# Performance work log

Measured on AMD Instinct MI355X. Metric: run time of the kernel, lower is better.

The kernel has to match this reference:

```python
import jax, jax.numpy as jnp
import numpy as np

N_AGENTS = 32
STATE_DIM = 512
EMBED = 64
BATCH = 32768


def setup_inputs() -> dict:
    key = jax.random.key(0)
    ks = jax.random.split(key, 16)
    g = lambda k, shape, fan_in: jax.random.normal(k, shape, jnp.float32) / np.sqrt(fan_in)
    return {
        "agent_qs": jax.random.normal(ks[0], (BATCH, N_AGENTS), jnp.float32),
        "states": jax.random.normal(ks[1], (BATCH, STATE_DIM), jnp.float32),
        # hyper_w1: Linear(state,E) -> ReLU -> Linear(E, n_agents*E)
        "w1_l1_w": g(ks[2], (EMBED, STATE_DIM), STATE_DIM),
        "w1_l1_b": jnp.zeros((EMBED,), jnp.float32),
        "w1_l2_w": g(ks[3], (N_AGENTS * EMBED, EMBED), EMBED),
        "w1_l2_b": jnp.zeros((N_AGENTS * EMBED,), jnp.float32),
        # hyper_w2: Linear(state,E) -> ReLU -> Linear(E, E)
        "w2_l1_w": g(ks[4], (EMBED, STATE_DIM), STATE_DIM),
        "w2_l1_b": jnp.zeros((EMBED,), jnp.float32),
        "w2_l2_w": g(ks[5], (EMBED, EMBED), EMBED),
        "w2_l2_b": jnp.zeros((EMBED,), jnp.float32),
        # hyper_b1: Linear(state, E)
        "b1_w": g(ks[6], (EMBED, STATE_DIM), STATE_DIM),
        "b1_b": jnp.zeros((EMBED,), jnp.float32),
        # hyper_b2: Linear(state,E) -> ReLU -> Linear(E, 1)
        "b2_l1_w": g(ks[7], (EMBED, STATE_DIM), STATE_DIM),
        "b2_l1_b": jnp.zeros((EMBED,), jnp.float32),
        "b2_l2_w": g(ks[8], (1, EMBED), EMBED),
        "b2_l2_b": jnp.zeros((1,), jnp.float32),
    }


def _linear(x, w, b):
    return x @ w.T + b


def reference(agent_qs, states,
              w1_l1_w, w1_l1_b, w1_l2_w, w1_l2_b,
              w2_l1_w, w2_l1_b, w2_l2_w, w2_l2_b,
              b1_w, b1_b, b2_l1_w, b2_l1_b, b2_l2_w, b2_l2_b):
    B = agent_qs.shape[0]
    # hypernetworks producing per-sample weights
    w1 = jnp.abs(_linear(jax.nn.relu(_linear(states, w1_l1_w, w1_l1_b)), w1_l2_w, w1_l2_b))
    w1 = w1.reshape(B, N_AGENTS, EMBED)                      # [B, A, E]
    b1 = _linear(states, b1_w, b1_b)                         # [B, E]
    hidden = jax.nn.elu(jnp.einsum('ba,bae->be', agent_qs, w1) + b1)  # [B, E]
    w2 = jnp.abs(_linear(jax.nn.relu(_linear(states, w2_l1_w, w2_l1_b)), w2_l2_w, w2_l2_b))  # [B, E]
    b2 = _linear(jax.nn.relu(_linear(states, b2_l1_w, b2_l1_b)), b2_l2_w, b2_l2_b)           # [B, 1]
    q_total = jnp.einsum('be,be->b', hidden, w2) + b2[:, 0]  # [B]
    return q_total
```

## Files before the change

kernel.cpp:

```cpp
#include <hip/hip_runtime.h>

typedef unsigned short u16;
typedef unsigned int u32;
typedef short bf16x8 __attribute__((ext_vector_type(8)));
typedef float f32x4 __attribute__((ext_vector_type(4)));
typedef u16 u16x4 __attribute__((ext_vector_type(4)));

#define NAG 32
#define STATE 512
#define EMBED 64
#define TB 64

#define OFF_W1L1 0
#define OFF_W2L1 32768
#define OFF_B1W  65536
#define OFF_B2L1 98304
#define OFF_W1L2 131072
#define OFF_W2L2 262144
#define WS_TOTAL 266240

__device__ __forceinline__ float bf2f(u16 u) {
    u32 i = ((u32)u) << 16; float f;
    __builtin_memcpy(&f, &i, 4); return f;
}
__device__ __forceinline__ u16 f2bf(float f) {
    u32 i; __builtin_memcpy(&i, &f, 4);
    return (u16)((i + 0x8000u) >> 16);
}
__device__ __forceinline__ bf16x8 ld8(const u16* p) {
    return *reinterpret_cast<const bf16x8*>(p);
}
__device__ __forceinline__ bf16x8 cvt8(f32x4 a, f32x4 b) {
    bf16x8 r;
#pragma unroll
    for (int i = 0; i < 4; ++i) r[i]     = (short)f2bf(a[i]);
#pragma unroll
    for (int i = 0; i < 4; ++i) r[i + 4] = (short)f2bf(b[i]);
    return r;
}

__global__ __launch_bounds__(256) void cvt_weights(
    const float* __restrict__ w1l1w, const float* __restrict__ w2l1w,
    const float* __restrict__ b1w,   const float* __restrict__ b2l1w,
    const float* __restrict__ w1l2w, const float* __restrict__ w2l2w,
    u16* __restrict__ ws)
{
    int idx = blockIdx.x * 256 + threadIdx.x;
    const float* src; int off;
    if      (idx < OFF_W2L1)  { src = w1l1w; off = OFF_W1L1; }
    else if (idx < OFF_B1W)   { src = w2l1w; off = OFF_W2L1; }
    else if (idx < OFF_B2L1)  { src = b1w;   off = OFF_B1W;  }
    else if (idx < OFF_W1L2)  { src = b2l1w; off = OFF_B2L1; }
    else if (idx < OFF_W2L2)  { src = w1l2w; off = OFF_W1L2; }
    else if (idx < WS_TOTAL)  { src = w2l2w; off = OFF_W2L2; }
    else return;
    ws[idx] = f2bf(src[idx - off]);
}

__global__ __launch_bounds__(256, 2) void qmix_kernel(
    const float* __restrict__ qs,    const float* __restrict__ st,
    const u16*  __restrict__ wsb,
    const float* __restrict__ w1l1b, const float* __restrict__ w1l2b,
    const float* __restrict__ w2l1b, const float* __restrict__ w2l2b,
    const float* __restrict__ b1b,   const float* __restrict__ b2l1b,
    const float* __restrict__ b2l2w, const float* __restrict__ b2l2b,
    float* __restrict__ out)
{
    __shared__ u16  y[TB][264];
    __shared__ u16  pbuf[4][TB][68];
    __shared__ u16  qst[NAG][68];
    __shared__ u16  w1bs[2048];
    __shared__ float qacc[TB];
    __shared__ float b2wv[64];

    const int t    = threadIdx.x;
    const int wave = t >> 6, lane = t & 63;
    const int m = lane & 15, quad = lane >> 4;
    const int sbase = blockIdx.x * TB;

    if (t < 64) b2wv[t] = b2l2w[t];
    {
        const float* qp = qs + (size_t)sbase * NAG + t * 8;
        f32x4 q0 = *reinterpret_cast<const f32x4*>(qp);
        f32x4 q1 = *reinterpret_cast<const f32x4*>(qp + 4);
        const int s = t >> 2, a0 = (t & 3) * 8;
#pragma unroll
        for (int j = 0; j < 4; ++j) qst[a0 + j][s]     = f2bf(q0[j]);
#pragma unroll
        for (int j = 0; j < 4; ++j) qst[a0 + 4 + j][s] = f2bf(q1[j]);
        f32x4 w0 = *reinterpret_cast<const f32x4*>(w1l2b + t * 8);
        f32x4 w1 = *reinterpret_cast<const f32x4*>(w1l2b + t * 8 + 4);
        *reinterpret_cast<bf16x8*>(&w1bs[t * 8]) = cvt8(w0, w1);
    }

    const u16*   wArow = wsb + (size_t)(wave * 64) * STATE;
    const float* stb   = st + (size_t)sbase * STATE;

    f32x4 acc[4][4] = {};
    for (int ks = 0; ks < 8; ++ks) {
        bf16x8 b[4][2];
#pragma unroll
        for (int ot = 0; ot < 4; ++ot) {
            const u16* wr = wArow + (size_t)(ot * 16 + m) * STATE + ks * 64 + quad * 8;
            b[ot][0] = ld8(wr);
            b[ot][1] = ld8(wr + 32);
        }
#pragma unroll
        for (int st2 = 0; st2 < 4; ++st2) {
            const float* ap = stb + (size_t)(st2 * 16 + m) * STATE + ks * 64 + quad * 8;
            f32x4 a0 = *reinterpret_cast<const f32x4*>(ap);
            f32x4 a1 = *reinterpret_cast<const f32x4*>(ap + 4);
            f32x4 a2 = *reinterpret_cast<const f32x4*>(ap + 32);
            f32x4 a3 = *reinterpret_cast<const f32x4*>(ap + 36);
            bf16x8 af0 = cvt8(a0, a1);
            bf16x8 af1 = cvt8(a2, a3);
#pragma unroll
            for (int ot = 0; ot < 4; ++ot)
                acc[st2][ot] = __builtin_amdgcn_mfma_f32_16x16x32_bf16(af0, b[ot][0], acc[st2][ot], 0, 0, 0);
#pragma unroll
            for (int ot = 0; ot < 4; ++ot)
                acc[st2][ot] = __builtin_amdgcn_mfma_f32_16x16x32_bf16(af1, b[ot][1], acc[st2][ot], 0, 0, 0);
        }
    }
    {
        const float* barr = (wave == 0) ? w1l1b : (wave == 1) ? w2l1b : (wave == 2) ? b1b : b2l1b;
        const bool isrelu = (wave != 2);
        float wb[4];
#pragma unroll
        for (int ot = 0; ot < 4; ++ot) wb[ot] = barr[ot * 16 + m];
#pragma unroll
        for (int st2 = 0; st2 < 4; ++st2)
#pragma unroll
            for (int ot = 0; ot < 4; ++ot)
#pragma unroll
                for (int r = 0; r < 4; ++r) {
                    float v = acc[st2][ot][r] + wb[ot];
                    if (isrelu) v = fmaxf(v, 0.f);
                    y[st2 * 16 + quad * 4 + r][wave * 64 + ot * 16 + m] = f2bf(v);
                }
    }
    __syncthreads();

    bf16x8 h1f[4][2];
#pragma unroll
    for (int st2 = 0; st2 < 4; ++st2) {
        h1f[st2][0] = *reinterpret_cast<const bf16x8*>(&y[st2 * 16 + m][quad * 8]);
        h1f[st2][1] = *reinterpret_cast<const bf16x8*>(&y[st2 * 16 + m][32 + quad * 8]);
    }

    f32x4 hacc[4][4] = {};
    for (int ag = 0; ag < 8; ++ag) {
        const int a = wave * 8 + ag;
        const u16* wp = wsb + OFF_W1L2 + (size_t)a * 64 * EMBED;
        bf16x8 b[4][2];
#pragma unroll
        for (int ot = 0; ot < 4; ++ot) {
            const u16* wr = wp + (size_t)(ot * 16 + m) * EMBED + quad * 8;
            b[ot][0] = ld8(wr);
            b[ot][1] = ld8(wr + 32);
        }
        float bias[4];
#pragma unroll
        for (int ot = 0; ot < 4; ++ot) bias[ot] = bf2f(w1bs[a * EMBED + ot * 16 + m]);
#pragma unroll
        for (int st2 = 0; st2 < 4; ++st2) {
            u16x4 qv = *reinterpret_cast<const u16x4*>(&qst[a][st2 * 16 + quad * 4]);
#pragma unroll
            for (int ot = 0; ot < 4; ++ot) {
                f32x4 p = {};
                p = __builtin_amdgcn_mfma_f32_16x16x32_bf16(h1f[st2][0], b[ot][0], p, 0, 0, 0);
                p = __builtin_amdgcn_mfma_f32_16x16x32_bf16(h1f[st2][1], b[ot][1], p, 0, 0, 0);
#pragma unroll
                for (int r = 0; r < 4; ++r)
                    hacc[st2][ot][r] += bf2f((u16)qv[r]) * fabsf(p[r] + bias[ot]);
            }
        }
    }
#pragma unroll
    for (int st2 = 0; st2 < 4; ++st2)
#pragma unroll
        for (int ot = 0; ot < 4; ++ot)
#pragma unroll
            for (int r = 0; r < 4; ++r)
                pbuf[wave][st2 * 16 + quad * 4 + r][ot * 16 + m] = f2bf(hacc[st2][ot][r]);
    __syncthreads();

    {
        const int s  = wave * 16 + (lane & 15);
        const int eb = (lane >> 4) * 16;
        float v[16];
#pragma unroll
        for (int j = 0; j < 16; ++j) v[j] = 0.f;
#pragma unroll
        for (int pw = 0; pw < 4; ++pw) {
#pragma unroll
            for (int c = 0; c < 4; ++c) {
                u16x4 x = *reinterpret_cast<const u16x4*>(&pbuf[pw][s][eb + c * 4]);
#pragma unroll
                for (int j = 0; j < 4; ++j) v[c * 4 + j] += bf2f((u16)x[j]);
            }
        }
        bf16x8 bv0 = *reinterpret_cast<const bf16x8*>(&y[s][128 + eb]);
        bf16x8 bv1 = *reinterpret_cast<const bf16x8*>(&y[s][128 + eb + 8]);
        bf16x8 o0, o1;
#pragma unroll
        for (int j = 0; j < 8; ++j) {
            float h0 = v[j] + bf2f((u16)bv0[j]);
            h0 = (h0 > 0.f) ? h0 : (__expf(h0) - 1.f);
            o0[j] = (short)f2bf(h0);
            float h1 = v[8 + j] + bf2f((u16)bv1[j]);
            h1 = (h1 > 0.f) ? h1 : (__expf(h1) - 1.f);
            o1[j] = (short)f2bf(h1);
        }
        *reinterpret_cast<bf16x8*>(&y[s][128 + eb])     = o0;
        *reinterpret_cast<bf16x8*>(&y[s][128 + eb + 8]) = o1;
    }
    __syncthreads();

    const int s0 = wave * 16;
    bf16x8 h2f0 = *reinterpret_cast<const bf16x8*>(&y[s0 + m][64 + quad * 8]);
    bf16x8 h2f1 = *reinterpret_cast<const bf16x8*>(&y[s0 + m][96 + quad * 8]);

    f32x4 qp = {};
#pragma unroll
    for (int tp = 0; tp < 4; ++tp) {
        const u16* wc = wsb + OFF_W2L2 + (size_t)(tp * 16 + m) * EMBED + quad * 8;
        bf16x8 b0 = ld8(wc);
        bf16x8 b1 = ld8(wc + 32);
        f32x4 p = {};
        p = __builtin_amdgcn_mfma_f32_16x16x32_bf16(h2f0, b0, p, 0, 0, 0);
        p = __builtin_amdgcn_mfma_f32_16x16x32_bf16(h2f1, b1, p, 0, 0, 0);
        const float bias = w2l2b[tp * 16 + m];
#pragma unroll
        for (int r = 0; r < 4; ++r)
            qp[r] += bf2f(y[s0 + quad * 4 + r][128 + tp * 16 + m]) * fabsf(p[r] + bias);
    }
#pragma unroll
    for (int off = 1; off < 16; off <<= 1) {
#pragma unroll
        for (int r = 0; r < 4; ++r) qp[r] += __shfl_xor(qp[r], off, 64);
    }
    if (m == 0) {
#pragma unroll
        for (int r = 0; r < 4; ++r) qacc[s0 + quad * 4 + r] = qp[r];
    }
    __syncthreads();

    if (t < TB) {
        float q = qacc[t] + b2l2b[0];
        float acc2 = 0.f;
#pragma unroll
        for (int kk = 0; kk < 8; ++kk) {
            bf16x8 hv = *reinterpret_cast<const bf16x8*>(&y[t][192 + kk * 8]);
#pragma unroll
            for (int j = 0; j < 8; ++j)
                acc2 += bf2f((u16)hv[j]) * b2wv[kk * 8 + j];
        }
        out[sbase + t] = q + acc2;
    }
}

extern "C" void kernel_launch(void* const* d_in, const int* in_sizes, int n_in,
                              void* d_out, int out_size, void* d_ws, size_t ws_size,
                              hipStream_t stream)
{
    const float* qs    = (const float*)d_in[0];
    const float* st    = (const float*)d_in[1];
    const float* w1l1w = (const float*)d_in[2];
    const float* w1l1b = (const float*)d_in[3];
    const float* w1l2w = (const float*)d_in[4];
    const float* w1l2b = (const float*)d_in[5];
    const float* w2l1w = (const float*)d_in[6];
    const float* w2l1b = (const float*)d_in[7];
    const float* w2l2w = (const float*)d_in[8];
    const float* w2l2b = (const float*)d_in[9];
    const float* b1w   = (const float*)d_in[10];
    const float* b1b   = (const float*)d_in[11];
    const float* b2l1w = (const float*)d_in[12];
    const float* b2l1b = (const float*)d_in[13];
    const float* b2l2w = (const float*)d_in[14];
    const float* b2l2b = (const float*)d_in[15];

    u16* wsb = (u16*)d_ws;

    cvt_weights<<<(WS_TOTAL + 255) / 256, 256, 0, stream>>>(
        w1l1w, w2l1w, b1w, b2l1w, w1l2w, w2l2w, wsb);

    int B = in_sizes[0] / NAG;
    int grid = B / TB;
    qmix_kernel<<<grid, 256, 0, stream>>>(
        qs, st, wsb,
        w1l1b, w1l2b, w2l1b, w2l2b, b1b, b2l1b, b2l2w, b2l2b,
        (float*)d_out);
}
```

Baseline: 175.3 us.

## Stage states tile through double-buffered LDS and prefetch weights in both GEMM loops

The states tile is now loaded cooperatively once per k-step, converted to bf16 and stored into a double-buffered LDS region. Previously each wave re-read and re-converted the whole states tile from global memory. Weight fragments for the first GEMM and for the per-agent w1 second layer are register double-buffered, so the next step's loads are in flight during the current MFMAs. The b2 hypernet dot product is folded into wave 3's epilogue with shuffle reductions, and shared memory is packed into one aliased buffer to cut LDS usage. The cost is a barrier per k-step and higher register pressure from the unrolled double buffers.

```diff
diff --git a/kernel.cpp b/kernel.cpp
--- a/kernel.cpp
+++ b/kernel.cpp
@@ -18,6 +18,21 @@
 #define OFF_W1L2 131072
 #define OFF_W2L2 262144
 #define WS_TOTAL 266240
+
+#define Y_STR    200
+#define SB_OFF   12800
+#define SB_STR   72
+#define SB_BUF   (64 * 72)
+#define W1BS_OFF 22016
+#define QST_OFF  24064
+#define QST_STR  68
+#define PBUF_OFF 12800
+#define PBUF_STR 68
+#define PBUF_WV  (64 * 68)
+#define QACC_OFF  30208
+#define QACC2_OFF 30336
+#define B2WV_OFF  30464
+#define SMEM_U16  30592
 
 __device__ __forceinline__ float bf2f(u16 u) {
     u32 i = ((u32)u) << 16; float f;
@@ -66,64 +81,97 @@
     const float* __restrict__ b2l2w, const float* __restrict__ b2l2b,
     float* __restrict__ out)
 {
-    __shared__ u16  y[TB][264];
-    __shared__ u16  pbuf[4][TB][68];
-    __shared__ u16  qst[NAG][68];
-    __shared__ u16  w1bs[2048];
-    __shared__ float qacc[TB];
-    __shared__ float b2wv[64];
+    __shared__ u16 smem[SMEM_U16];
+    float* qaccF  = (float*)(smem + QACC_OFF);
+    float* qacc2F = (float*)(smem + QACC2_OFF);
+    float* b2wvF  = (float*)(smem + B2WV_OFF);
 
     const int t    = threadIdx.x;
     const int wave = t >> 6, lane = t & 63;
     const int m = lane & 15, quad = lane >> 4;
     const int sbase = blockIdx.x * TB;
 
-    if (t < 64) b2wv[t] = b2l2w[t];
+    if (t < 64) b2wvF[t] = b2l2w[t];
     {
         const float* qp = qs + (size_t)sbase * NAG + t * 8;
         f32x4 q0 = *reinterpret_cast<const f32x4*>(qp);
         f32x4 q1 = *reinterpret_cast<const f32x4*>(qp + 4);
         const int s = t >> 2, a0 = (t & 3) * 8;
 #pragma unroll
-        for (int j = 0; j < 4; ++j) qst[a0 + j][s]     = f2bf(q0[j]);
-#pragma unroll
-        for (int j = 0; j < 4; ++j) qst[a0 + 4 + j][s] = f2bf(q1[j]);
+        for (int j = 0; j < 4; ++j) smem[QST_OFF + (a0 + j) * QST_STR + s]     = f2bf(q0[j]);
+#pragma unroll
+        for (int j = 0; j < 4; ++j) smem[QST_OFF + (a0 + 4 + j) * QST_STR + s] = f2bf(q1[j]);
         f32x4 w0 = *reinterpret_cast<const f32x4*>(w1l2b + t * 8);
         f32x4 w1 = *reinterpret_cast<const f32x4*>(w1l2b + t * 8 + 4);
-        *reinterpret_cast<bf16x8*>(&w1bs[t * 8]) = cvt8(w0, w1);
-    }
-
-    const u16*   wArow = wsb + (size_t)(wave * 64) * STATE;
-    const float* stb   = st + (size_t)sbase * STATE;
+        *reinterpret_cast<bf16x8*>(&smem[W1BS_OFF + t * 8]) = cvt8(w0, w1);
+    }
+
+    const int ss1 = t >> 3, c8 = t & 7;
+    const float* stb = st + (size_t)sbase * STATE;
+
+    {
+        const float* g1 = stb + (size_t)ss1 * STATE + c8 * 8;
+        const float* g2 = g1 + (size_t)32 * STATE;
+        f32x4 a0 = *reinterpret_cast<const f32x4*>(g1);
+        f32x4 a1 = *reinterpret_cast<const f32x4*>(g1 + 4);
+        f32x4 a2 = *reinterpret_cast<const f32x4*>(g2);
+        f32x4 a3 = *reinterpret_cast<const f32x4*>(g2 + 4);
+        u16* dst = smem + SB_OFF;
+        *reinterpret_cast<bf16x8*>(&dst[ss1 * SB_STR + c8 * 8])        = cvt8(a0, a1);
+        *reinterpret_cast<bf16x8*>(&dst[(ss1 + 32) * SB_STR + c8 * 8]) = cvt8(a2, a3);
+    }
+
+    const u16* wAw = wsb + (size_t)(wave * 64) * STATE;
+    bf16x8 bfr[2][4][2];
+#pragma unroll
+    for (int ot = 0; ot < 4; ++ot) {
+        const u16* wr = wAw + (size_t)(ot * 16 + m) * STATE + quad * 8;
+        bfr[0][ot][0] = ld8(wr);
+        bfr[0][ot][1] = ld8(wr + 32);
+    }
+    __syncthreads();
 
     f32x4 acc[4][4] = {};
+#pragma unroll
     for (int ks = 0; ks < 8; ++ks) {
-        bf16x8 b[4][2];
-#pragma unroll
-        for (int ot = 0; ot < 4; ++ot) {
-            const u16* wr = wArow + (size_t)(ot * 16 + m) * STATE + ks * 64 + quad * 8;
-            b[ot][0] = ld8(wr);
-            b[ot][1] = ld8(wr + 32);
-        }
+        f32x4 sa0 = {}, sa1 = {}, sa2 = {}, sa3 = {};
+        if (ks < 7) {
+            const float* g1 = stb + (size_t)ss1 * STATE + (ks + 1) * 64 + c8 * 8;
+            const float* g2 = g1 + (size_t)32 * STATE;
+            sa0 = *reinterpret_cast<const f32x4*>(g1);
+            sa1 = *reinterpret_cast<const f32x4*>(g1 + 4);
+            sa2 = *reinterpret_cast<const f32x4*>(g2);
+            sa3 = *reinterpret_cast<const f32x4*>(g2 + 4);
+#pragma unroll
+            for (int ot = 0; ot < 4; ++ot) {
+                const u16* wr = wAw + (size_t)(ot * 16 + m) * STATE + (ks + 1) * 64 + quad * 8;
+                bfr[(ks + 1) & 1][ot][0] = ld8(wr);
+                bfr[(ks + 1) & 1][ot][1] = ld8(wr + 32);
+            }
+        }
+        const u16* sbc = smem + SB_OFF + (ks & 1) * SB_BUF;
 #pragma unroll
         for (int st2 = 0; st2 < 4; ++st2) {
-            const float* ap = stb + (size_t)(st2 * 16 + m) * STATE + ks * 64 + quad * 8;
-            f32x4 a0 = *reinterpret_cast<const f32x4*>(ap);
-            f32x4 a1 = *reinterpret_cast<const f32x4*>(ap + 4);
-            f32x4 a2 = *reinterpret_cast<const f32x4*>(ap + 32);
-            f32x4 a3 = *reinterpret_cast<const f32x4*>(ap + 36);
-            bf16x8 af0 = cvt8(a0, a1);
-            bf16x8 af1 = cvt8(a2, a3);
+            const int row = st2 * 16 + m;
+            bf16x8 af0 = ld8(&sbc[row * SB_STR + quad * 8]);
+            bf16x8 af1 = ld8(&sbc[row * SB_STR + (quad + 4) * 8]);
 #pragma unroll
             for (int ot = 0; ot < 4; ++ot)
-                acc[st2][ot] = __builtin_amdgcn_mfma_f32_16x16x32_bf16(af0, b[ot][0], acc[st2][ot], 0, 0, 0);
+                acc[st2][ot] = __builtin_amdgcn_mfma_f32_16x16x32_bf16(af0, bfr[ks & 1][ot][0], acc[st2][ot], 0, 0, 0);
 #pragma unroll
             for (int ot = 0; ot < 4; ++ot)
-                acc[st2][ot] = __builtin_amdgcn_mfma_f32_16x16x32_bf16(af1, b[ot][1], acc[st2][ot], 0, 0, 0);
-        }
-    }
-    {
-        const float* barr = (wave == 0) ? w1l1b : (wave == 1) ? w2l1b : (wave == 2) ? b1b : b2l1b;
+                acc[st2][ot] = __builtin_amdgcn_mfma_f32_16x16x32_bf16(af1, bfr[ks & 1][ot][1], acc[st2][ot], 0, 0, 0);
+        }
+        if (ks < 7) {
+            u16* dst = smem + SB_OFF + ((ks + 1) & 1) * SB_BUF;
+            *reinterpret_cast<bf16x8*>(&dst[ss1 * SB_STR + c8 * 8])        = cvt8(sa0, sa1);
+            *reinterpret_cast<bf16x8*>(&dst[(ss1 + 32) * SB_STR + c8 * 8]) = cvt8(sa2, sa3);
+        }
+        __syncthreads();
+    }
+
+    if (wave != 3) {
+        const float* barr = (wave == 0) ? w1l1b : (wave == 1) ? w2l1b : b1b;
         const bool isrelu = (wave != 2);
         float wb[4];
 #pragma unroll
@@ -136,53 +184,84 @@
                 for (int r = 0; r < 4; ++r) {
                     float v = acc[st2][ot][r] + wb[ot];
                     if (isrelu) v = fmaxf(v, 0.f);
-                    y[st2 * 16 + quad * 4 + r][wave * 64 + ot * 16 + m] = f2bf(v);
+                    smem[(st2 * 16 + quad * 4 + r) * Y_STR + wave * 64 + ot * 16 + m] = f2bf(v);
                 }
+    } else {
+        float wb[4], bw[4];
+#pragma unroll
+        for (int ot = 0; ot < 4; ++ot) wb[ot] = b2l1b[ot * 16 + m];
+#pragma unroll
+        for (int ot = 0; ot < 4; ++ot) bw[ot] = b2wvF[ot * 16 + m];
+#pragma unroll
+        for (int st2 = 0; st2 < 4; ++st2)
+#pragma unroll
+            for (int r = 0; r < 4; ++r) {
+                float pd = 0.f;
+#pragma unroll
+                for (int ot = 0; ot < 4; ++ot)
+                    pd += fmaxf(acc[st2][ot][r] + wb[ot], 0.f) * bw[ot];
+#pragma unroll
+                for (int off = 1; off < 16; off <<= 1) pd += __shfl_xor(pd, off, 64);
+                if (m == 0) qacc2F[st2 * 16 + quad * 4 + r] = pd;
+            }
     }
     __syncthreads();
 
     bf16x8 h1f[4][2];
 #pragma unroll
     for (int st2 = 0; st2 < 4; ++st2) {
-        h1f[st2][0] = *reinterpret_cast<const bf16x8*>(&y[st2 * 16 + m][quad * 8]);
-        h1f[st2][1] = *reinterpret_cast<const bf16x8*>(&y[st2 * 16 + m][32 + quad * 8]);
+        h1f[st2][0] = ld8(&smem[(st2 * 16 + m) * Y_STR + quad * 8]);
+        h1f[st2][1] = ld8(&smem[(st2 * 16 + m) * Y_STR + 32 + quad * 8]);
+    }
+
+    const u16* wB = wsb + OFF_W1L2 + (size_t)(wave * 8) * 64 * EMBED;
+    bf16x8 bb[2][4][2];
+#pragma unroll
+    for (int ot = 0; ot < 4; ++ot) {
+        const u16* wr = wB + (size_t)(ot * 16 + m) * EMBED + quad * 8;
+        bb[0][ot][0] = ld8(wr);
+        bb[0][ot][1] = ld8(wr + 32);
     }
 
     f32x4 hacc[4][4] = {};
+#pragma unroll
     for (int ag = 0; ag < 8; ++ag) {
+        if (ag < 7) {
+#pragma unroll
+            for (int ot = 0; ot < 4; ++ot) {
+                const u16* wr = wB + (size_t)((ag + 1) * 64 + ot * 16 + m) * EMBED + quad * 8;
+                bb[(ag + 1) & 1][ot][0] = ld8(wr);
+                bb[(ag + 1) & 1][ot][1] = ld8(wr + 32);
+            }
+        }
         const int a = wave * 8 + ag;
-        const u16* wp = wsb + OFF_W1L2 + (size_t)a * 64 * EMBED;
-        bf16x8 b[4][2];
-#pragma unroll
-        for (int ot = 0; ot < 4; ++ot) {
-            const u16* wr = wp + (size_t)(ot * 16 + m) * EMBED + quad * 8;
-            b[ot][0] = ld8(wr);
-            b[ot][1] = ld8(wr + 32);
-        }
         float bias[4];
 #pragma unroll
-        for (int ot = 0; ot < 4; ++ot) bias[ot] = bf2f(w1bs[a * EMBED + ot * 16 + m]);
+        for (int ot = 0; ot < 4; ++ot) bias[ot] = bf2f(smem[W1BS_OFF + a * EMBED + ot * 16 + m]);
 #pragma unroll
         for (int st2 = 0; st2 < 4; ++st2) {
-            u16x4 qv = *reinterpret_cast<const u16x4*>(&qst[a][st2 * 16 + quad * 4]);
+            u16x4 qv = *reinterpret_cast<const u16x4*>(&smem[QST_OFF + a * QST_STR + st2 * 16 + quad * 4]);
 #pragma unroll
             for (int ot = 0; ot < 4; ++ot) {
                 f32x4 p = {};
-                p = __builtin_amdgcn_mfma_f32_16x16x32_bf16(h1f[st2][0], b[ot][0], p, 0, 0, 0);
-                p = __builtin_amdgcn_mfma_f32_16x16x32_bf16(h1f[st2][1], b[ot][1], p, 0, 0, 0);
+                p = __builtin_amdgcn_mfma_f32_16x16x32_bf16(h1f[st2][0], bb[ag & 1][ot][0], p, 0, 0, 0);
+                p = __builtin_amdgcn_mfma_f32_16x16x32_bf16(h1f[st2][1], bb[ag & 1][ot][1], p, 0, 0, 0);
 #pragma unroll
                 for (int r = 0; r < 4; ++r)
                     hacc[st2][ot][r] += bf2f((u16)qv[r]) * fabsf(p[r] + bias[ot]);
             }
         }
     }
+    __syncthreads();
+
 #pragma unroll
     for (int st2 = 0; st2 < 4; ++st2)
 #pragma unroll
         for (int ot = 0; ot < 4; ++ot)
 #pragma unroll
             for (int r = 0; r < 4; ++r)
-                pbuf[wave][st2 * 16 + quad * 4 + r][ot * 16 + m] = f2bf(hacc[st2][ot][r]);
+                smem[PBUF_OFF + wave * PBUF_WV + (st2 * 16 + quad * 4 + r) * PBUF_STR + ot * 16 + m]
+                    = f2bf(hacc[st2][ot][r]);
     __syncthreads();
 
     {
@@ -195,13 +274,14 @@
         for (int pw = 0; pw < 4; ++pw) {
 #pragma unroll
             for (int c = 0; c < 4; ++c) {
-                u16x4 x = *reinterpret_cast<const u16x4*>(&pbuf[pw][s][eb + c * 4]);
+                u16x4 x = *reinterpret_cast<const u16x4*>(
+                    &smem[PBUF_OFF + pw * PBUF_WV + s * PBUF_STR + eb + c * 4]);
 #pragma unroll
                 for (int j = 0; j < 4; ++j) v[c * 4 + j] += bf2f((u16)x[j]);
             }
         }
-        bf16x8 bv0 = *reinterpret_cast<const bf16x8*>(&y[s][128 + eb]);
-        bf16x8 bv1 = *reinterpret_cast<const bf16x8*>(&y[s][128 + eb + 8]);
+        bf16x8 bv0 = ld8(&smem[s * Y_STR + 128 + eb]);
+        bf16x8 bv1 = ld8(&smem[s * Y_STR + 128 + eb + 8]);
         bf16x8 o0, o1;
 #pragma unroll
         for (int j = 0; j < 8; ++j) {
@@ -212,28 +292,28 @@
             h1 = (h1 > 0.f) ? h1 : (__expf(h1) - 1.f);
             o1[j] = (short)f2bf(h1);
         }
-        *reinterpret_cast<bf16x8*>(&y[s][128 + eb])     = o0;
-        *reinterpret_cast<bf16x8*>(&y[s][128 + eb + 8]) = o1;
+        *reinterpret_cast<bf16x8*>(&smem[s * Y_STR + 128 + eb])     = o0;
+        *reinterpret_cast<bf16x8*>(&smem[s * Y_STR + 128 + eb + 8]) = o1;
     }
     __syncthreads();
 
     const int s0 = wave * 16;
-    bf16x8 h2f0 = *reinterpret_cast<const bf16x8*>(&y[s0 + m][64 + quad * 8]);
-    bf16x8 h2f1 = *reinterpret_cast<const bf16x8*>(&y[s0 + m][96 + quad * 8]);
+    bf16x8 h2f0 = ld8(&smem[(s0 + m) * Y_STR + 64 + quad * 8]);
+    bf16x8 h2f1 = ld8(&smem[(s0 + m) * Y_STR + 96 + quad * 8]);
 
     f32x4 qp = {};
 #pragma unroll
     for (int tp = 0; tp < 4; ++tp) {
         const u16* wc = wsb + OFF_W2L2 + (size_t)(tp * 16 + m) * EMBED + quad * 8;
-        bf16x8 b0 = ld8(wc);
-        bf16x8 b1 = ld8(wc + 32);
+        bf16x8 c0 = ld8(wc);
+        bf16x8 c1 = ld8(wc + 32);
         f32x4 p = {};
-        p = __builtin_amdgcn_mfma_f32_16x16x32_bf16(h2f0, b0, p, 0, 0, 0);
-        p = __builtin_amdgcn_mfma_f32_16x16x32_bf16(h2f1, b1, p, 0, 0, 0);
+        p = __builtin_amdgcn_mfma_f32_16x16x32_bf16(h2f0, c0, p, 0, 0, 0);
+        p = __builtin_amdgcn_mfma_f32_16x16x32_bf16(h2f1, c1, p, 0, 0, 0);
         const float bias = w2l2b[tp * 16 + m];
 #pragma unroll
         for (int r = 0; r < 4; ++r)
-            qp[r] += bf2f(y[s0 + quad * 4 + r][128 + tp * 16 + m]) * fabsf(p[r] + bias);
+            qp[r] += bf2f(smem[(s0 + quad * 4 + r) * Y_STR + 128 + tp * 16 + m]) * fabsf(p[r] + bias);
     }
 #pragma unroll
     for (int off = 1; off < 16; off <<= 1) {
@@ -242,22 +322,11 @@
     }
     if (m == 0) {
 #pragma unroll
-        for (int r = 0; r < 4; ++r) qacc[s0 + quad * 4 + r] = qp[r];
-    }
-    __syncthreads();
-
-    if (t < TB) {
-        float q = qacc[t] + b2l2b[0];
-        float acc2 = 0.f;
-#pragma unroll
-        for (int kk = 0; kk < 8; ++kk) {
-            bf16x8 hv = *reinterpret_cast<const bf16x8*>(&y[t][192 + kk * 8]);
-#pragma unroll
-            for (int j = 0; j < 8; ++j)
-                acc2 += bf2f((u16)hv[j]) * b2wv[kk * 8 + j];
-        }
-        out[sbase + t] = q + acc2;
-    }
+        for (int r = 0; r < 4; ++r) qaccF[s0 + quad * 4 + r] = qp[r];
+    }
+    __syncthreads();
+
+    if (t < TB) out[sbase + t] = qaccF[t] + qacc2F[t] + b2l2b[0];
 }
 
 extern "C" void kernel_launch(void* const* d_in, const int* in_sizes, int n_in,
```

Measured after the change: 157.3 us. 1.11x faster.
